# Kernel tuning notes

Measured on AMD Instinct MI355X. Metric: run time of the kernel, lower is better.

## Reference

```python
import jax, jax.numpy as jnp
import numpy as np

N_NODES = 20000
NC = 16
NUM_BASIS = 5
MAX_CENTER = 3.5

# Real-basis Clebsch-Gordan tensors C[m, m_f, m_o] for the (l, l_f) -> l_o paths.
# Real l=1 basis ordered (m=-1,0,1) = (y,z,x); (y,z,x) is a cyclic permutation of
# (x,y,z) so the standard Levi-Civita gives the 1x1->1 coupling.
_C000 = np.ones((1, 1, 1), dtype=np.float32)
_C011 = np.eye(3, dtype=np.float32).reshape(1, 3, 3)
_C101 = np.eye(3, dtype=np.float32).reshape(3, 1, 3)
_C110 = (np.eye(3, dtype=np.float32) / np.sqrt(3.0)).reshape(3, 3, 1)
_eps = np.zeros((3, 3, 3), dtype=np.float32)
for (i, j, k) in [(0, 1, 2), (1, 2, 0), (2, 0, 1)]:
    _eps[i, j, k] = 1.0
    _eps[i, k, j] = -1.0
_C111 = (_eps / np.sqrt(2.0)).astype(np.float32)

Y00 = 0.28209479177387814  # 1 / (2 sqrt(pi))
Y1C = 0.4886025119029199   # sqrt(3 / (4 pi))


def _spherical_filter(edges, coeffs, l_f):
    """SphericalFilter.__call__: RBF radial part x solid harmonics. -> [E, n_c, 2l_f+1]."""
    centers = jnp.linspace(0.0, MAX_CENTER, NUM_BASIS)
    spread = (MAX_CENTER - 0.0) / NUM_BASIS  # (max - min) / num_basis = 0.7
    radius = jnp.linalg.norm(edges, ord=2, axis=-1)              # [E]
    rbfs = jnp.exp(-spread * (radius[:, None] - centers) ** 2)   # [E, num_basis]
    rad = rbfs @ coeffs.T                                        # [E, n_c]
    if l_f == 0:
        y = jnp.full(edges.shape[:-1] + (1,), Y00, dtype=edges.dtype)
    else:  # l_f == 1: solid harmonics r^1 * Y_1m, order (y, z, x)
        y = Y1C * edges[:, jnp.array([1, 2, 0])]
    y = jnp.nan_to_num(y)
    return rad[:, :, None] * y[:, None, :]


def _tp(nodes, filt, cg, w):
    """Depthwise CG tensor product: [E,c,m],[E,c,f],[m,f,o] -> w[c] * [E,c,o]."""
    out = jnp.einsum('ecm,ecf,mfo->eco', nodes, filt, jnp.asarray(cg))
    return w[None, :, None] * out


def setup_inputs() -> dict:
    key = jax.random.key(0)
    ks = jax.random.split(key, 16)
    E = 640000
    inp = {
        'coords': jax.random.normal(ks[0], (N_NODES, 3), dtype=jnp.float32),
        'nodes0': jax.random.normal(ks[1], (N_NODES, NC, 1), dtype=jnp.float32),
        'nodes1': jax.random.normal(ks[2], (N_NODES, NC, 3), dtype=jnp.float32),
        'edges': jax.random.normal(ks[3], (E, 3), dtype=jnp.float32),
        'senders': jax.random.randint(ks[4], (E,), 0, N_NODES, dtype=jnp.int32),
        'receivers': jax.random.randint(ks[5], (E,), 0, N_NODES, dtype=jnp.int32),
        'coeffs_00': jax.random.uniform(ks[6], (NC, NUM_BASIS), dtype=jnp.float32),
        'coeffs_01': jax.random.uniform(ks[7], (NC, NUM_BASIS), dtype=jnp.float32),
        'coeffs_10': jax.random.uniform(ks[8], (NC, NUM_BASIS), dtype=jnp.float32),
        'coeffs_11': jax.random.uniform(ks[9], (NC, NUM_BASIS), dtype=jnp.float32),
        'w_000': jax.random.normal(ks[10], (NC,), dtype=jnp.float32) + 1.0,
        'w_011': jax.random.normal(ks[11], (NC,), dtype=jnp.float32) + 1.0,
        'w_101': jax.random.normal(ks[12], (NC,), dtype=jnp.float32) + 1.0,
        'w_110': jax.random.normal(ks[13], (NC,), dtype=jnp.float32) + 1.0,
        'w_111': jax.random.normal(ks[14], (NC,), dtype=jnp.float32) + 1.0,
    }
    return inp


def reference(coords, nodes0, nodes1, edges, senders, receivers,
              coeffs_00, coeffs_01, coeffs_10, coeffs_11,
              w_000, w_011, w_101, w_110, w_111):
    # Gather sender node features once per l.
    n0s = nodes0[senders]  # [E, NC, 1]
    n1s = nodes1[senders]  # [E, NC, 3]

    # Filters (loop order: l=0 filters [l_f=0, l_f=1], then l=1 filters).
    f00 = _spherical_filter(edges, coeffs_00, 0)  # [E, NC, 1]
    f01 = _spherical_filter(edges, coeffs_01, 1)  # [E, NC, 3]
    f10 = _spherical_filter(edges, coeffs_10, 0)  # [E, NC, 1]
    f11 = _spherical_filter(edges, coeffs_11, 1)  # [E, NC, 3]

    # Tensor-product messages, concatenated per output degree along channels.
    # l_o = 0 paths: (l=0, l_f=0), (l=1, l_f=1)
    m0 = jnp.concatenate([
        _tp(n0s, f00, _C000, w_000),
        _tp(n1s, f11, _C110, w_110),
    ], axis=-2)  # [E, 2*NC, 1]
    # l_o = 1 paths: (0,1), (1,0), (1,1)
    m1 = jnp.concatenate([
        _tp(n0s, f01, _C011, w_011),
        _tp(n1s, f10, _C101, w_101),
        _tp(n1s, f11, _C111, w_111),
    ], axis=-2)  # [E, 3*NC, 3]

    new0 = jax.ops.segment_sum(m0, receivers, num_segments=N_NODES)
    new1 = jax.ops.segment_sum(m1, receivers, num_segments=N_NODES)
    return coords, new0, new1
```

## Files before the change

kernel.cpp:

```cpp
#include <hip/hip_runtime.h>
#include <hip/hip_fp16.h>

#define E_EDGES 640000
#define NN 20000
#define NC 16
#define PBIN 64

#define Y00F 0.28209479177387814f
#define Y1CF 0.4886025119029199f
#define RS3  0.5773502691896258f
#define RS2  0.7071067811865476f

typedef float nf4 __attribute__((ext_vector_type(4)));
typedef unsigned int nu2 __attribute__((ext_vector_type(2)));

__device__ __forceinline__ unsigned pack2h(float a, float b) {
    unsigned short ua = __half_as_ushort(__float2half(a));
    unsigned short ub = __half_as_ushort(__float2half(b));
    return (unsigned)ua | ((unsigned)ub << 16);
}
__device__ __forceinline__ float lo_h(unsigned u) {
    return __half2float(__ushort_as_half((unsigned short)(u & 0xffffu)));
}
__device__ __forceinline__ float hi_h(unsigned u) {
    return __half2float(__ushort_as_half((unsigned short)(u >> 16)));
}


__global__ void init1_kernel(const float* __restrict__ coords,
                             const float* __restrict__ nodes0,
                             const float* __restrict__ nodes1,
                             float* __restrict__ out,
                             int* __restrict__ cnt,
                             int* __restrict__ ovf_count,
                             nu2* __restrict__ nodes_h) {
    int i = blockIdx.x * blockDim.x + threadIdx.x;
    if (i < 3 * NN) out[i] = coords[i];
    if (i < NN) cnt[i] = 0;
    if (i == 0) *ovf_count = 0;
    if (i < NN * NC) {
        float n0 = nodes0[i];
        const float* n1p = nodes1 + i * 3;
        nu2 v;
        v.x = pack2h(n0, n1p[0]);
        v.y = pack2h(n1p[1], n1p[2]);
        nodes_h[i] = v;
    }
}

__global__ void bin_kernel(const float* __restrict__ edges,
                           const int* __restrict__ senders,
                           const int* __restrict__ receivers,
                           int* __restrict__ cnt,
                           nf4* __restrict__ bins,
                           int* __restrict__ ovf_count,
                           int* __restrict__ ovf_list) {
    int e = blockIdx.x * blockDim.x + threadIdx.x;
    if (e >= E_EDGES) return;
    float ex = edges[3 * e + 0];
    float ey = edges[3 * e + 1];
    float ez = edges[3 * e + 2];
    int s  = senders[e];
    int rc = receivers[e];
    int pos = atomicAdd(&cnt[rc], 1);
    if (pos < PBIN) {
        float r2 = ex * ex + ey * ey + ez * ez;
        float r  = sqrtf(r2);
        float A  = __expf(-0.7f * r2);
        float t  = __expf(1.225f * r);
        nf4 rec;
        rec.x = __uint_as_float(pack2h(Y1CF * ey, Y1CF * ez));
        rec.y = __uint_as_float(pack2h(Y1CF * ex, t));
        rec.z = A;
        rec.w = __int_as_float(s);
        bins[(size_t)rc * PBIN + pos] = rec;
    } else {
        int k = atomicAdd(ovf_count, 1);
        if (k < 4096) ovf_list[k] = e;
    }
}

__global__ __launch_bounds__(256) void gather1_kernel(
    const nf4*    __restrict__ bins,
    const int*    __restrict__ cnt,
    const nu2*    __restrict__ nodes_h,
    const float*  __restrict__ c00, const float* __restrict__ c01,
    const float*  __restrict__ c10, const float* __restrict__ c11,
    const float*  __restrict__ w000, const float* __restrict__ w011,
    const float*  __restrict__ w101, const float* __restrict__ w110,
    const float*  __restrict__ w111,
    float* __restrict__ out0, float* __restrict__ out1)
{
    int t    = threadIdx.x;
    int slot = t >> 7;
    int node = blockIdx.x * 2 + slot;
    int tid  = t & 127;
    int c    = tid & 15;
    int j    = tid >> 4;

    const float KB[5] = {1.0f, 0.58512723f, 0.11721218f, 0.00803909f, 1.8876652e-4f};
    float k00[5], k01[5], k10[5], k11[5];
#pragma unroll
    for (int b = 0; b < 5; b++) {
        k00[b] = c00[c * 5 + b] * KB[b];
        k01[b] = c01[c * 5 + b] * KB[b];
        k10[b] = c10[c * 5 + b] * KB[b];
        k11[b] = c11[c * 5 + b] * KB[b];
    }

    int n = cnt[node];
    n = (n < PBIN) ? n : PBIN;
    const nf4* base = bins + (size_t)node * PBIN;

    float a000 = 0.f, a110 = 0.f;
    float a011x = 0.f, a011y = 0.f, a011z = 0.f;
    float a101x = 0.f, a101y = 0.f, a101z = 0.f;
    float a111x = 0.f, a111y = 0.f, a111z = 0.f;

#define HORNER(k, t) fmaf((t), fmaf((t), fmaf((t), fmaf((t), k[4], k[3]), k[2]), k[1]), k[0])
#define BODY(rec)                                                          \
    {                                                                      \
        unsigned u0 = __float_as_uint(rec.x);                              \
        unsigned u1 = __float_as_uint(rec.y);                              \
        float py = lo_h(u0), pz = hi_h(u0);                                \
        float px = lo_h(u1), tf = hi_h(u1);                                \
        float Af = rec.z;                                                  \
        int s = __float_as_int(rec.w);                                     \
        nu2 nh = nodes_h[s * NC + c];                                      \
        float rad00 = Af * HORNER(k00, tf);                                \
        float rad01 = Af * HORNER(k01, tf);                                \
        float rad10 = Af * HORNER(k10, tf);                                \
        float rad11 = Af * HORNER(k11, tf);                                \
        float n0  = lo_h(nh.x), n1a = hi_h(nh.x);                          \
        float n1b = lo_h(nh.y), n1c = hi_h(nh.y);                          \
        a000 = fmaf(n0, rad00, a000);                                      \
        a110 = fmaf(rad11, n1a * py + n1b * pz + n1c * px, a110);          \
        float kA = n0 * rad01;                                             \
        a011x = fmaf(kA, py, a011x);                                       \
        a011y = fmaf(kA, pz, a011y);                                       \
        a011z = fmaf(kA, px, a011z);                                       \
        a101x = fmaf(rad10, n1a, a101x);                                   \
        a101y = fmaf(rad10, n1b, a101y);                                   \
        a101z = fmaf(rad10, n1c, a101z);                                   \
        a111x = fmaf(rad11, n1b * px - n1c * pz, a111x);                   \
        a111y = fmaf(rad11, n1c * py - n1a * px, a111y);                   \
        a111z = fmaf(rad11, n1a * pz - n1b * py, a111z);                   \
    }

    int i = j;
    for (; i + 8 < n; i += 16) {
        nf4 r0 = __builtin_nontemporal_load(&base[i]);
        nf4 r1 = __builtin_nontemporal_load(&base[i + 8]);
        BODY(r0);
        BODY(r1);
    }
    if (i < n) {
        nf4 r0 = __builtin_nontemporal_load(&base[i]);
        BODY(r0);
    }
#undef BODY
#undef HORNER

#define RED(v) v += __shfl_xor(v, 16, 64); v += __shfl_xor(v, 32, 64)
    RED(a000); RED(a110);
    RED(a011x); RED(a011y); RED(a011z);
    RED(a101x); RED(a101y); RED(a101z);
    RED(a111x); RED(a111y); RED(a111z);
#undef RED

    __shared__ float red[2][16][11];
    int half = tid >> 6;
    if (half == 0 && (tid & 63) < 16) {
        float* p = red[slot][c];
        p[0] = a000;  p[1] = a110;
        p[2] = a011x; p[3] = a011y; p[4]  = a011z;
        p[5] = a101x; p[6] = a101y; p[7]  = a101z;
        p[8] = a111x; p[9] = a111y; p[10] = a111z;
    }
    __syncthreads();
    if (half == 1 && (tid & 63) < 16) {
        const float* p = red[slot][c];
        a000  += p[0];  a110  += p[1];
        a011x += p[2];  a011y += p[3];  a011z += p[4];
        a101x += p[5];  a101y += p[6];  a101z += p[7];
        a111x += p[8];  a111y += p[9];  a111z += p[10];

        float s000 = w000[c] * Y00F;
        float s110 = w110[c] * RS3;
        float s011 = w011[c];
        float s101 = w101[c] * Y00F;
        float s111 = w111[c] * RS2;

        out0[node * 32 + c]      = s000 * a000;
        out0[node * 32 + 16 + c] = s110 * a110;

        float* o1 = out1 + node * 144;
        o1[3 * c + 0] = s011 * a011x;
        o1[3 * c + 1] = s011 * a011y;
        o1[3 * c + 2] = s011 * a011z;
        o1[3 * (16 + c) + 0] = s101 * a101x;
        o1[3 * (16 + c) + 1] = s101 * a101y;
        o1[3 * (16 + c) + 2] = s101 * a101z;
        o1[3 * (32 + c) + 0] = s111 * a111x;
        o1[3 * (32 + c) + 1] = s111 * a111y;
        o1[3 * (32 + c) + 2] = s111 * a111z;
    }
}

__global__ void cleanup_kernel(
    const int* __restrict__ ovf_count, const int* __restrict__ ovf_list,
    const float* __restrict__ edges, const int* __restrict__ senders,
    const int* __restrict__ receivers,
    const float* __restrict__ nodes0, const float* __restrict__ nodes1,
    const float* __restrict__ c00, const float* __restrict__ c01,
    const float* __restrict__ c10, const float* __restrict__ c11,
    const float* __restrict__ w000, const float* __restrict__ w011,
    const float* __restrict__ w101, const float* __restrict__ w110,
    const float* __restrict__ w111,
    float* __restrict__ out0, float* __restrict__ out1)
{
    int nov = *ovf_count;
    if (nov > 4096) nov = 4096;
    for (int k = threadIdx.x; k < nov; k += blockDim.x) {
        int e = ovf_list[k];
        float ex = edges[3 * e + 0], ey = edges[3 * e + 1], ez = edges[3 * e + 2];
        float r = sqrtf(ex * ex + ey * ey + ez * ez);
        float rbf[5];
#pragma unroll
        for (int b = 0; b < 5; b++) {
            float d = r - 0.875f * (float)b;
            rbf[b] = __expf(-0.7f * d * d);
        }
        int s = senders[e], rc = receivers[e];
        const float* n0p = nodes0 + s * NC;
        const float* n1p = nodes1 + s * NC * 3;
        float* o0 = out0 + rc * 32;
        float* o1 = out1 + rc * 144;
        float pey = Y1CF * ey, pez = Y1CF * ez, pex = Y1CF * ex;
        for (int c = 0; c < NC; c++) {
            float rad00 = 0.f, rad01 = 0.f, rad10 = 0.f, rad11 = 0.f;
#pragma unroll
            for (int b = 0; b < 5; b++) {
                rad00 = fmaf(rbf[b], c00[c * 5 + b], rad00);
                rad01 = fmaf(rbf[b], c01[c * 5 + b], rad01);
                rad10 = fmaf(rbf[b], c10[c * 5 + b], rad10);
                rad11 = fmaf(rbf[b], c11[c * 5 + b], rad11);
            }
            float n0 = n0p[c];
            float n1a = n1p[3 * c + 0], n1b = n1p[3 * c + 1], n1c = n1p[3 * c + 2];
            float f11a = rad11 * pey, f11b = rad11 * pez, f11c = rad11 * pex;
            atomicAdd(&o0[c], w000[c] * n0 * rad00 * Y00F);
            atomicAdd(&o0[16 + c], w110[c] * RS3 * (n1a * f11a + n1b * f11b + n1c * f11c));
            float kA = w011[c] * n0 * rad01;
            atomicAdd(&o1[3 * c + 0], kA * pey);
            atomicAdd(&o1[3 * c + 1], kA * pez);
            atomicAdd(&o1[3 * c + 2], kA * pex);
            float kB = w101[c] * rad10 * Y00F;
            atomicAdd(&o1[3 * (16 + c) + 0], kB * n1a);
            atomicAdd(&o1[3 * (16 + c) + 1], kB * n1b);
            atomicAdd(&o1[3 * (16 + c) + 2], kB * n1c);
            float kC = w111[c] * RS2;
            atomicAdd(&o1[3 * (32 + c) + 0], kC * (n1b * f11c - n1c * f11b));
            atomicAdd(&o1[3 * (32 + c) + 1], kC * (n1c * f11a - n1a * f11c));
            atomicAdd(&o1[3 * (32 + c) + 2], kC * (n1a * f11b - n1b * f11a));
        }
    }
}

__global__ void init_out_fb(const float* __restrict__ coords,
                            float* __restrict__ out, int out_size) {
    int i = blockIdx.x * blockDim.x + threadIdx.x;
    if (i < 3 * NN) out[i] = coords[i];
    else if (i < out_size) out[i] = 0.0f;
}

__global__ __launch_bounds__(256) void tp_edges_fb(
    const float* __restrict__ edges, const int* __restrict__ senders,
    const int* __restrict__ receivers, const float* __restrict__ nodes0,
    const float* __restrict__ nodes1,
    const float* __restrict__ c00, const float* __restrict__ c01,
    const float* __restrict__ c10, const float* __restrict__ c11,
    const float* __restrict__ w000, const float* __restrict__ w011,
    const float* __restrict__ w101, const float* __restrict__ w110,
    const float* __restrict__ w111,
    float* __restrict__ out0, float* __restrict__ out1) {
    int e = blockIdx.x * blockDim.x + threadIdx.x;
    if (e >= E_EDGES) return;
    float ex = edges[3 * e + 0], ey = edges[3 * e + 1], ez = edges[3 * e + 2];
    float r = sqrtf(ex * ex + ey * ey + ez * ez);
    float rbf[5];
#pragma unroll
    for (int b = 0; b < 5; b++) {
        float d = r - 0.875f * (float)b;
        rbf[b] = __expf(-0.7f * d * d);
    }
    int s = senders[e], rc = receivers[e];
    const float* n0p = nodes0 + s * NC;
    const float* n1p = nodes1 + s * NC * 3;
    float* o0 = out0 + rc * 32;
    float* o1 = out1 + rc * 144;
    float pey = Y1CF * ey, pez = Y1CF * ez, pex = Y1CF * ex;
    for (int c = 0; c < NC; c++) {
        float rad00 = 0.f, rad01 = 0.f, rad10 = 0.f, rad11 = 0.f;
#pragma unroll
        for (int b = 0; b < 5; b++) {
            rad00 = fmaf(rbf[b], c00[c * 5 + b], rad00);
            rad01 = fmaf(rbf[b], c01[c * 5 + b], rad01);
            rad10 = fmaf(rbf[b], c10[c * 5 + b], rad10);
            rad11 = fmaf(rbf[b], c11[c * 5 + b], rad11);
        }
        float n0 = n0p[c];
        float n1a = n1p[3 * c + 0], n1b = n1p[3 * c + 1], n1c = n1p[3 * c + 2];
        float f11a = rad11 * pey, f11b = rad11 * pez, f11c = rad11 * pex;
        atomicAdd(&o0[c], w000[c] * n0 * rad00 * Y00F);
        atomicAdd(&o0[16 + c], w110[c] * RS3 * (n1a * f11a + n1b * f11b + n1c * f11c));
        float kA = w011[c] * n0 * rad01;
        atomicAdd(&o1[3 * c + 0], kA * pey);
        atomicAdd(&o1[3 * c + 1], kA * pez);
        atomicAdd(&o1[3 * c + 2], kA * pex);
        float kB = w101[c] * rad10 * Y00F;
        atomicAdd(&o1[3 * (16 + c) + 0], kB * n1a);
        atomicAdd(&o1[3 * (16 + c) + 1], kB * n1b);
        atomicAdd(&o1[3 * (16 + c) + 2], kB * n1c);
        float kC = w111[c] * RS2;
        atomicAdd(&o1[3 * (32 + c) + 0], kC * (n1b * f11c - n1c * f11b));
        atomicAdd(&o1[3 * (32 + c) + 1], kC * (n1c * f11a - n1a * f11c));
        atomicAdd(&o1[3 * (32 + c) + 2], kC * (n1a * f11b - n1b * f11a));
    }
}

extern "C" void kernel_launch(void* const* d_in, const int* in_sizes, int n_in,
                              void* d_out, int out_size, void* d_ws, size_t ws_size,
                              hipStream_t stream) {
    const float* coords    = (const float*)d_in[0];
    const float* nodes0    = (const float*)d_in[1];
    const float* nodes1    = (const float*)d_in[2];
    const float* edges     = (const float*)d_in[3];
    const int*   senders   = (const int*)  d_in[4];
    const int*   receivers = (const int*)  d_in[5];
    const float* c00       = (const float*)d_in[6];
    const float* c01       = (const float*)d_in[7];
    const float* c10       = (const float*)d_in[8];
    const float* c11       = (const float*)d_in[9];
    const float* w000      = (const float*)d_in[10];
    const float* w011      = (const float*)d_in[11];
    const float* w101      = (const float*)d_in[12];
    const float* w110      = (const float*)d_in[13];
    const float* w111      = (const float*)d_in[14];

    float* out  = (float*)d_out;
    float* out0 = out + 3 * NN;
    float* out1 = out + 3 * NN + NN * 2 * NC;

    size_t bins_bytes  = (size_t)NN * PBIN * 16;
    size_t nodes_bytes = (size_t)NN * NC * 8;
    size_t need1 = bins_bytes + nodes_bytes + (size_t)(NN + 1 + 4096) * 4;

    if (ws_size >= need1) {
        nf4* bins      = (nf4*)d_ws;
        nu2* nodes_h   = (nu2*)((char*)d_ws + bins_bytes);
        int* cnt       = (int*)((char*)d_ws + bins_bytes + nodes_bytes);
        int* ovf_count = cnt + NN;
        int* ovf_list  = ovf_count + 1;

        init1_kernel<<<(NN * NC + 255) / 256, 256, 0, stream>>>(
            coords, nodes0, nodes1, out, cnt, ovf_count, nodes_h);
        bin_kernel<<<(E_EDGES + 255) / 256, 256, 0, stream>>>(
            edges, senders, receivers, cnt, bins, ovf_count, ovf_list);
        gather1_kernel<<<NN / 2, 256, 0, stream>>>(
            bins, cnt, nodes_h,
            c00, c01, c10, c11, w000, w011, w101, w110, w111, out0, out1);
        cleanup_kernel<<<1, 256, 0, stream>>>(
            ovf_count, ovf_list, edges, senders, receivers, nodes0, nodes1,
            c00, c01, c10, c11, w000, w011, w101, w110, w111, out0, out1);
    } else {
        init_out_fb<<<(out_size + 255) / 256, 256, 0, stream>>>(coords, out, out_size);
        tp_edges_fb<<<(E_EDGES + 255) / 256, 256, 0, stream>>>(
            edges, senders, receivers, nodes0, nodes1,
            c00, c01, c10, c11, w000, w011, w101, w110, w111, out0, out1);
    }
}
```

Measured before the change: 165.4 us.

## Shrink bin records to 8 bytes and recompute radial terms in gather

Each binned edge record shrinks from 16 to 8 bytes by storing the raw edge vector as fp16 and packing the sender index into the upper 16 bits of the second word. The radius and both exponentials are now recomputed in the gather kernel from the fp16 edge components. The Y1 constant moves into the per-channel output scales. This halves bin write and read traffic at the cost of more ALU work per edge per channel in the gather. Sender indices up to 20000 fit in 16 bits, but the fp16 rounding of the edge vector now feeds the exponentials, which changes numerical error.

```diff
diff --git a/kernel.cpp b/kernel.cpp
--- a/kernel.cpp
+++ b/kernel.cpp
@@ -52,7 +52,7 @@
                            const int* __restrict__ senders,
                            const int* __restrict__ receivers,
                            int* __restrict__ cnt,
-                           nf4* __restrict__ bins,
+                           nu2* __restrict__ bins,
                            int* __restrict__ ovf_count,
                            int* __restrict__ ovf_list) {
     int e = blockIdx.x * blockDim.x + threadIdx.x;
@@ -64,15 +64,9 @@
     int rc = receivers[e];
     int pos = atomicAdd(&cnt[rc], 1);
     if (pos < PBIN) {
-        float r2 = ex * ex + ey * ey + ez * ez;
-        float r  = sqrtf(r2);
-        float A  = __expf(-0.7f * r2);
-        float t  = __expf(1.225f * r);
-        nf4 rec;
-        rec.x = __uint_as_float(pack2h(Y1CF * ey, Y1CF * ez));
-        rec.y = __uint_as_float(pack2h(Y1CF * ex, t));
-        rec.z = A;
-        rec.w = __int_as_float(s);
+        nu2 rec;
+        rec.x = pack2h(ey, ez);
+        rec.y = (unsigned)__half_as_ushort(__float2half(ex)) | ((unsigned)s << 16);
         bins[(size_t)rc * PBIN + pos] = rec;
     } else {
         int k = atomicAdd(ovf_count, 1);
@@ -81,7 +75,7 @@
 }
 
 __global__ __launch_bounds__(256) void gather1_kernel(
-    const nf4*    __restrict__ bins,
+    const nu2*    __restrict__ bins,
     const int*    __restrict__ cnt,
     const nu2*    __restrict__ nodes_h,
     const float*  __restrict__ c00, const float* __restrict__ c01,
@@ -110,7 +104,7 @@
 
     int n = cnt[node];
     n = (n < PBIN) ? n : PBIN;
-    const nf4* base = bins + (size_t)node * PBIN;
+    const nu2* base = bins + (size_t)node * PBIN;
 
     float a000 = 0.f, a110 = 0.f;
     float a011x = 0.f, a011y = 0.f, a011z = 0.f;
@@ -118,15 +112,14 @@
     float a111x = 0.f, a111y = 0.f, a111z = 0.f;
 
 #define HORNER(k, t) fmaf((t), fmaf((t), fmaf((t), fmaf((t), k[4], k[3]), k[2]), k[1]), k[0])
-#define BODY(rec)                                                          \
+#define COMPUTE(rec, nh)                                                   \
     {                                                                      \
-        unsigned u0 = __float_as_uint(rec.x);                              \
-        unsigned u1 = __float_as_uint(rec.y);                              \
-        float py = lo_h(u0), pz = hi_h(u0);                                \
-        float px = lo_h(u1), tf = hi_h(u1);                                \
-        float Af = rec.z;                                                  \
-        int s = __float_as_int(rec.w);                                     \
-        nu2 nh = nodes_h[s * NC + c];                                      \
+        float py = lo_h(rec.x), pz = hi_h(rec.x);                          \
+        float px = lo_h(rec.y);                                            \
+        float r2 = fmaf(px, px, fmaf(py, py, pz * pz));                    \
+        float r  = sqrtf(r2);                                              \
+        float Af = __expf(-0.7f * r2);                                     \
+        float tf = __expf(1.225f * r);                                     \
         float rad00 = Af * HORNER(k00, tf);                                \
         float rad01 = Af * HORNER(k01, tf);                                \
         float rad10 = Af * HORNER(k10, tf);                                \
@@ -149,16 +142,22 @@
 
     int i = j;
     for (; i + 8 < n; i += 16) {
-        nf4 r0 = __builtin_nontemporal_load(&base[i]);
-        nf4 r1 = __builtin_nontemporal_load(&base[i + 8]);
-        BODY(r0);
-        BODY(r1);
+        nu2 r0 = __builtin_nontemporal_load(&base[i]);
+        nu2 r1 = __builtin_nontemporal_load(&base[i + 8]);
+        int s0 = r0.y >> 16;
+        int s1 = r1.y >> 16;
+        nu2 nh0 = nodes_h[s0 * NC + c];
+        nu2 nh1 = nodes_h[s1 * NC + c];
+        COMPUTE(r0, nh0);
+        COMPUTE(r1, nh1);
     }
     if (i < n) {
-        nf4 r0 = __builtin_nontemporal_load(&base[i]);
-        BODY(r0);
-    }
-#undef BODY
+        nu2 r0 = __builtin_nontemporal_load(&base[i]);
+        int s0 = r0.y >> 16;
+        nu2 nh0 = nodes_h[s0 * NC + c];
+        COMPUTE(r0, nh0);
+    }
+#undef COMPUTE
 #undef HORNER
 
 #define RED(v) v += __shfl_xor(v, 16, 64); v += __shfl_xor(v, 32, 64)
@@ -186,10 +185,10 @@
         a111x += p[8];  a111y += p[9];  a111z += p[10];
 
         float s000 = w000[c] * Y00F;
-        float s110 = w110[c] * RS3;
-        float s011 = w011[c];
+        float s110 = w110[c] * RS3 * Y1CF;
+        float s011 = w011[c] * Y1CF;
         float s101 = w101[c] * Y00F;
-        float s111 = w111[c] * RS2;
+        float s111 = w111[c] * RS2 * Y1CF;
 
         out0[node * 32 + c]      = s000 * a000;
         out0[node * 32 + 16 + c] = s110 * a110;
@@ -352,12 +351,12 @@
     float* out0 = out + 3 * NN;
     float* out1 = out + 3 * NN + NN * 2 * NC;
 
-    size_t bins_bytes  = (size_t)NN * PBIN * 16;
+    size_t bins_bytes  = (size_t)NN * PBIN * 8;
     size_t nodes_bytes = (size_t)NN * NC * 8;
     size_t need1 = bins_bytes + nodes_bytes + (size_t)(NN + 1 + 4096) * 4;
 
     if (ws_size >= need1) {
-        nf4* bins      = (nf4*)d_ws;
+        nu2* bins      = (nu2*)d_ws;
         nu2* nodes_h   = (nu2*)((char*)d_ws + bins_bytes);
         int* cnt       = (int*)((char*)d_ws + bins_bytes + nodes_bytes);
         int* ovf_count = cnt + NN;
```

Result: no change. 165.8 us (+0.3%).
